# Kernel tuning notes

Hardware: AMD Instinct MI355X
Metric: run time of the kernel (lower is better)

## Reference

```python
import jax, jax.numpy as jnp
import numpy as np

N = 4096
D = 512   # d_model == dff (required by the original code path)
H = 4
NEG = -1e10
ALPHA = 0.3  # keras LeakyReLU default alpha


def setup_inputs() -> dict:
    key = jax.random.key(0)
    ks = jax.random.split(key, 8)
    nodes = jax.random.normal(ks[0], (N, D), dtype=jnp.float32)
    # sparse-ish 0/1 dense adjacency with self loops
    adj = (jax.random.uniform(ks[1], (N, N)) < 0.01).astype(jnp.float32)
    adj = jnp.maximum(adj, jnp.eye(N, dtype=jnp.float32))
    s = 0.05
    W_node = jax.random.normal(ks[2], (D, D), dtype=jnp.float32) * s
    b_node = jnp.zeros((D,), dtype=jnp.float32)
    K = jax.random.normal(ks[3], (H, D, D), dtype=jnp.float32) * s
    A_self = jax.random.normal(ks[4], (H, D), dtype=jnp.float32) * s
    A_neigh = jax.random.normal(ks[5], (H, D), dtype=jnp.float32) * s
    return {"nodes": nodes, "adj": adj, "W_node": W_node, "b_node": b_node,
            "K": K, "A_self": A_self, "A_neigh": A_neigh, "num_heads": H}


def reference(nodes, adj, W_node, b_node, K, A_self, A_neigh, num_heads):
    # node_layer: Dense(dff)
    x = nodes @ W_node + b_node                       # [N, D]
    # per-head projection, vectorized over heads
    feats = jnp.einsum('nd,hdf->hnf', x, K)           # [H, N, D]
    # additive attention scores; both terms are per-row scalars -> [H, N]
    s = jnp.einsum('hnf,hf->hn', feats, A_self) + jnp.einsum('hnf,hf->hn', feats, A_neigh)
    s = jnp.where(s > 0, s, ALPHA * s)                # LeakyReLU(alpha=0.3)
    # broadcast row score over columns + adjacency mask, softmax over neighbors
    logits = s[:, :, None] + NEG * (1.0 - adj)[None]  # [H, N, N]
    attn = jax.nn.softmax(logits, axis=-1)
    # dropout is identity at inference (training=False)
    out = jnp.einsum('hij,hjf->hif', attn, feats)     # [H, N, D]
    out = jnp.mean(out, axis=0)                       # mean over heads
    return jax.nn.relu(out)
```

## Files before the change

kernel.cpp:

```cpp
#include <hip/hip_runtime.h>


typedef short  short8 __attribute__((ext_vector_type(8)));
typedef float  f32x4  __attribute__((ext_vector_type(4)));

__device__ inline unsigned short f2bf(float f) {
    union { float f; unsigned int u; } v; v.f = f;
    unsigned int u = v.u;
    u += 0x7fffu + ((u >> 16) & 1u);
    return (unsigned short)(u >> 16);
}

__device__ inline void gl_lds16(const void* gp, void* lp) {
    __builtin_amdgcn_global_load_lds(
        (const __attribute__((address_space(1))) void*)gp,
        (__attribute__((address_space(3))) void*)lp, 16, 0, 0);
}

__global__ __launch_bounds__(256) void prep_kernel(
        const float* __restrict__ nodes, const float* __restrict__ adj,
        const float* __restrict__ W, const float* __restrict__ b,
        const float* __restrict__ K,
        unsigned short* __restrict__ MmatT, float* __restrict__ bias2,
        unsigned short* __restrict__ nodesBf,
        int* __restrict__ degArr, int* __restrict__ nbrArr,
        int N, int D, int H, int numCast) {
    __shared__ unsigned short As[64][32];
    __shared__ unsigned short Bs[64][32];
    __shared__ float red[4][64];
    __shared__ int lst[1024];
    __shared__ int cnt;

    const int bid = blockIdx.x;
    const int tid = threadIdx.x;
    const int DD  = D * D;
    const int lane = tid & 63, wave = tid >> 6;
    const int wy = wave >> 1, wx = wave & 1;
    const int l15 = lane & 15, quad = lane >> 4;

    if (bid < 64) {
        const int by = bid >> 3, bx = bid & 7;
        const int f0 = by * 64, d0 = bx * 64;
        const float invH = 1.0f / (float)H;
        const int kk = tid >> 3;
        const int ff = (tid & 7) * 8;
        const int dr = tid >> 2;
        const int dk = (tid & 3) * 8;
        f32x4 acc[2][2] = {};
        for (int k0 = 0; k0 < D; k0 += 32) {
            float s[8] = {0.f, 0.f, 0.f, 0.f, 0.f, 0.f, 0.f, 0.f};
            for (int h = 0; h < H; ++h) {
                const float* kp = K + ((size_t)h * D + (k0 + kk)) * D + f0 + ff;
                float4 x = *reinterpret_cast<const float4*>(kp);
                float4 y = *reinterpret_cast<const float4*>(kp + 4);
                s[0] += x.x; s[1] += x.y; s[2] += x.z; s[3] += x.w;
                s[4] += y.x; s[5] += y.y; s[6] += y.z; s[7] += y.w;
            }
            const float* wp = W + (size_t)(d0 + dr) * D + k0 + dk;
            float4 u = *reinterpret_cast<const float4*>(wp);
            float4 v = *reinterpret_cast<const float4*>(wp + 4);
            short8 bv;
            bv[0] = (short)f2bf(u.x); bv[1] = (short)f2bf(u.y);
            bv[2] = (short)f2bf(u.z); bv[3] = (short)f2bf(u.w);
            bv[4] = (short)f2bf(v.x); bv[5] = (short)f2bf(v.y);
            bv[6] = (short)f2bf(v.z); bv[7] = (short)f2bf(v.w);
            __syncthreads();
#pragma unroll
            for (int j = 0; j < 8; ++j)
                As[ff + j][kk] = f2bf(s[j] * invH);
            *reinterpret_cast<short8*>(&Bs[dr][dk]) = bv;
            __syncthreads();
            short8 a0 = *reinterpret_cast<const short8*>(&As[wy * 32 +      l15][quad * 8]);
            short8 a1 = *reinterpret_cast<const short8*>(&As[wy * 32 + 16 + l15][quad * 8]);
            short8 b0 = *reinterpret_cast<const short8*>(&Bs[wx * 32 +      l15][quad * 8]);
            short8 b1 = *reinterpret_cast<const short8*>(&Bs[wx * 32 + 16 + l15][quad * 8]);
            acc[0][0] = __builtin_amdgcn_mfma_f32_16x16x32_bf16(a0, b0, acc[0][0], 0, 0, 0);
            acc[0][1] = __builtin_amdgcn_mfma_f32_16x16x32_bf16(a0, b1, acc[0][1], 0, 0, 0);
            acc[1][0] = __builtin_amdgcn_mfma_f32_16x16x32_bf16(a1, b0, acc[1][0], 0, 0, 0);
            acc[1][1] = __builtin_amdgcn_mfma_f32_16x16x32_bf16(a1, b1, acc[1][1], 0, 0, 0);
        }
#pragma unroll
        for (int mi = 0; mi < 2; ++mi)
#pragma unroll
            for (int ni = 0; ni < 2; ++ni) {
                int col = d0 + wx * 32 + ni * 16 + l15;
#pragma unroll
                for (int r = 0; r < 4; ++r) {
                    int row = f0 + wy * 32 + mi * 16 + quad * 4 + r;
                    MmatT[(size_t)row * D + col] = f2bf(acc[mi][ni][r]);
                }
            }
    } else if (bid < 72) {
        const int f0 = (bid - 64) * 64;
        const int fl = tid & 63, grp = tid >> 6;
        const float invH = 1.0f / (float)H;
        float a = 0.f;
        for (int d = grp; d < D; d += 4) {
            const float* kp = K + (size_t)d * D + f0 + fl;
            float v = 0.f;
#pragma unroll
            for (int h = 0; h < 4; ++h) v += kp[(size_t)h * DD];
            a += b[d] * v;
        }
        red[grp][fl] = a;
        __syncthreads();
        if (tid < 64)
            bias2[f0 + tid] = (red[0][tid] + red[1][tid] + red[2][tid] + red[3][tid]) * invH;
    } else if (bid < 72 + N) {
        const int row = bid - 72;
        if (tid == 0) cnt = 0;
        __syncthreads();
        const float* arow = adj + (size_t)row * N;
        const int nper = N >> 8;
        const int base = tid * nper;
        const float4* ap = reinterpret_cast<const float4*>(arow + base);
        for (int c = 0; c < (nper >> 2); ++c) {
            float4 a = ap[c];
            int b4 = base + c * 4;
            if (a.x > 0.5f) { int p = atomicAdd(&cnt, 1); if (p < 1024) lst[p] = b4;     }
            if (a.y > 0.5f) { int p = atomicAdd(&cnt, 1); if (p < 1024) lst[p] = b4 + 1; }
            if (a.z > 0.5f) { int p = atomicAdd(&cnt, 1); if (p < 1024) lst[p] = b4 + 2; }
            if (a.w > 0.5f) { int p = atomicAdd(&cnt, 1); if (p < 1024) lst[p] = b4 + 3; }
        }
        __syncthreads();
        int deg = cnt; if (deg > 1024) deg = 1024;
        if (tid == 0) degArr[row] = deg;
        for (int i = tid; i < deg; i += 256)
            nbrArr[(size_t)row * 1024 + i] = lst[i];
    } else {
        const int total  = (N * D) >> 3;
        const int stride = numCast << 8;
        for (int i = (bid - 72 - N) * 256 + tid; i < total; i += stride) {
            const float* p = nodes + (size_t)i * 8;
            float4 x = *reinterpret_cast<const float4*>(p);
            float4 y = *reinterpret_cast<const float4*>(p + 4);
            short8 o;
            o[0] = (short)f2bf(x.x); o[1] = (short)f2bf(x.y);
            o[2] = (short)f2bf(x.z); o[3] = (short)f2bf(x.w);
            o[4] = (short)f2bf(y.x); o[5] = (short)f2bf(y.y);
            o[6] = (short)f2bf(y.z); o[7] = (short)f2bf(y.w);
            *reinterpret_cast<short8*>(nodesBf + (size_t)i * 8) = o;
        }
    }
}

__global__ __launch_bounds__(256) void gemm2_kernel(
        const unsigned short* __restrict__ nodesBf,
        const unsigned short* __restrict__ MmatT,
        const float* __restrict__ bias2, unsigned short* __restrict__ g, int D) {
    __shared__ unsigned short As[2][64][32];
    __shared__ unsigned short Bs[2][64][32];
    const int bid = blockIdx.x;
    const int by = bid >> 3, bx = bid & 7;
    const int tid = threadIdx.x;
    const int lane = tid & 63, wave = tid >> 6;
    const int wy = wave >> 1, wx = wave & 1;
    const int l15 = lane & 15, quad = lane >> 4;

    const unsigned short* Ag = nodesBf + (size_t)(by * 64 + (tid >> 2)) * D + (tid & 3) * 8;
    const unsigned short* Bg = MmatT   + (size_t)(bx * 64 + (tid >> 2)) * D + (tid & 3) * 8;
    unsigned short* AsW0 = &As[0][0][0] + wave * 512;
    unsigned short* AsW1 = &As[1][0][0] + wave * 512;
    unsigned short* BsW0 = &Bs[0][0][0] + wave * 512;
    unsigned short* BsW1 = &Bs[1][0][0] + wave * 512;

    f32x4 acc[2][2] = {};
    gl_lds16(Ag, AsW0);
    gl_lds16(Bg, BsW0);

    int cur = 0;
#pragma unroll
    for (int k0 = 0; k0 < 512; k0 += 32) {
        if (k0 + 32 < 512) {
            gl_lds16(Ag + k0 + 32, cur ? AsW0 : AsW1);
            gl_lds16(Bg + k0 + 32, cur ? BsW0 : BsW1);
            asm volatile("s_waitcnt vmcnt(2)" ::: "memory");
        } else {
            asm volatile("s_waitcnt vmcnt(0)" ::: "memory");
        }
        __builtin_amdgcn_s_barrier();
        __builtin_amdgcn_sched_barrier(0);
        const unsigned short (*A)[32] = cur ? As[1] : As[0];
        const unsigned short (*B)[32] = cur ? Bs[1] : Bs[0];
        short8 a0 = *reinterpret_cast<const short8*>(&A[wy * 32 +      l15][quad * 8]);
        short8 a1 = *reinterpret_cast<const short8*>(&A[wy * 32 + 16 + l15][quad * 8]);
        short8 b0 = *reinterpret_cast<const short8*>(&B[wx * 32 +      l15][quad * 8]);
        short8 b1 = *reinterpret_cast<const short8*>(&B[wx * 32 + 16 + l15][quad * 8]);
        acc[0][0] = __builtin_amdgcn_mfma_f32_16x16x32_bf16(a0, b0, acc[0][0], 0, 0, 0);
        acc[0][1] = __builtin_amdgcn_mfma_f32_16x16x32_bf16(a0, b1, acc[0][1], 0, 0, 0);
        acc[1][0] = __builtin_amdgcn_mfma_f32_16x16x32_bf16(a1, b0, acc[1][0], 0, 0, 0);
        acc[1][1] = __builtin_amdgcn_mfma_f32_16x16x32_bf16(a1, b1, acc[1][1], 0, 0, 0);
        __builtin_amdgcn_sched_barrier(0);
        asm volatile("s_waitcnt lgkmcnt(0)" ::: "memory");
        __builtin_amdgcn_s_barrier();
        cur ^= 1;
    }

#pragma unroll
    for (int mi = 0; mi < 2; ++mi)
#pragma unroll
        for (int ni = 0; ni < 2; ++ni) {
            int col = bx * 64 + wx * 32 + ni * 16 + l15;
            float bvl = bias2[col];
#pragma unroll
            for (int r = 0; r < 4; ++r) {
                int row = by * 64 + wy * 32 + mi * 16 + quad * 4 + r;
                g[(size_t)row * D + col] = f2bf(acc[mi][ni][r] + bvl);
            }
        }
}

__global__ __launch_bounds__(256) void aggregate_kernel(
        const int* __restrict__ degArr, const int* __restrict__ nbrArr,
        const unsigned short* __restrict__ g, float* __restrict__ out,
        int N, int D) {
    const int row = blockIdx.x;
    const int tid = threadIdx.x;
    __shared__ int lst[1024];
    const int deg = degArr[row];
    for (int i = tid; i < deg; i += 256) lst[i] = nbrArr[(size_t)row * 1024 + i];
    __syncthreads();

    const int col = tid * 2;
    float acc0 = 0.f, acc1 = 0.f;
    int k = 0;
    for (; k + 8 <= deg; k += 8) {
        unsigned int u[8];
#pragma unroll
        for (int j = 0; j < 8; ++j)
            u[j] = *reinterpret_cast<const unsigned int*>(&g[(size_t)lst[k + j] * D + col]);
#pragma unroll
        for (int j = 0; j < 8; ++j) {
            union { unsigned int i; float f; } lo, hi;
            lo.i = u[j] << 16; hi.i = u[j] & 0xffff0000u;
            acc0 += lo.f; acc1 += hi.f;
        }
    }
    for (; k < deg; ++k) {
        unsigned int u = *reinterpret_cast<const unsigned int*>(&g[(size_t)lst[k] * D + col]);
        union { unsigned int i; float f; } lo, hi;
        lo.i = u << 16; hi.i = u & 0xffff0000u;
        acc0 += lo.f; acc1 += hi.f;
    }

    float inv = deg > 0 ? 1.f / (float)deg : 0.f;
    acc0 *= inv; acc1 *= inv;
    float2 o;
    o.x = acc0 > 0.f ? acc0 : 0.f;
    o.y = acc1 > 0.f ? acc1 : 0.f;
    *reinterpret_cast<float2*>(&out[(size_t)row * D + col]) = o;
}

extern "C" void kernel_launch(void* const* d_in, const int* in_sizes, int n_in,
                              void* d_out, int out_size, void* d_ws, size_t ws_size,
                              hipStream_t stream) {
    const float* nodes  = (const float*)d_in[0];
    const float* adj    = (const float*)d_in[1];
    const float* W_node = (const float*)d_in[2];
    const float* b_node = (const float*)d_in[3];
    const float* K      = (const float*)d_in[4];

    const int D  = in_sizes[3];
    const int N  = in_sizes[0] / D;
    const int H  = in_sizes[4] / (D * D);
    const int DD = D * D;

    float* out = (float*)d_out;

    char* ws = (char*)d_ws;
    unsigned short* MmatT   = (unsigned short*)(ws);
    size_t off = (size_t)DD * 2;
    float*          bias2   = (float*)(ws + off);          off += (size_t)D * 4;
    unsigned short* nodesBf = (unsigned short*)(ws + off); off += (size_t)N * D * 2;
    unsigned short* g_bf16  = (unsigned short*)(ws + off); off += (size_t)N * D * 2;
    int*            degArr  = (int*)(ws + off);            off += (size_t)N * 4;
    int*            nbrArr  = (int*)(ws + off);

    const int numCast = 952;
    prep_kernel<<<dim3(64 + 8 + N + numCast), 256, 0, stream>>>(
        nodes, adj, W_node, b_node, K, MmatT, bias2, nodesBf, degArr, nbrArr,
        N, D, H, numCast);

    gemm2_kernel<<<dim3((N / 64) * (D / 64)), 256, 0, stream>>>(
        nodesBf, MmatT, bias2, g_bf16, D);

    aggregate_kernel<<<dim3(N), 256, 0, stream>>>(degArr, nbrArr, g_bf16, out, N, D);
}
```

Before: 168.2 us.

## Pad and swizzle LDS tiles, prefetch weights, coalesce adjacency scan, remap blocks

```diff
diff --git a/kernel.cpp b/kernel.cpp
--- a/kernel.cpp
+++ b/kernel.cpp
@@ -25,8 +25,8 @@
         unsigned short* __restrict__ nodesBf,
         int* __restrict__ degArr, int* __restrict__ nbrArr,
         int N, int D, int H, int numCast) {
-    __shared__ unsigned short As[64][32];
-    __shared__ unsigned short Bs[64][32];
+    __shared__ unsigned short As[64][40];
+    __shared__ unsigned short Bs[64][40];
     __shared__ float red[4][64];
     __shared__ int lst[1024];
     __shared__ int cnt;
@@ -46,24 +46,47 @@
         const int ff = (tid & 7) * 8;
         const int dr = tid >> 2;
         const int dk = (tid & 3) * 8;
+
+        float4 kc[4][2], wc[2];
+#pragma unroll
+        for (int h = 0; h < 4; ++h) {
+            const float* kp = K + ((size_t)h * D + kk) * D + f0 + ff;
+            kc[h][0] = *reinterpret_cast<const float4*>(kp);
+            kc[h][1] = *reinterpret_cast<const float4*>(kp + 4);
+        }
+        {
+            const float* wp = W + (size_t)(d0 + dr) * D + dk;
+            wc[0] = *reinterpret_cast<const float4*>(wp);
+            wc[1] = *reinterpret_cast<const float4*>(wp + 4);
+        }
+
         f32x4 acc[2][2] = {};
-        for (int k0 = 0; k0 < D; k0 += 32) {
-            float s[8] = {0.f, 0.f, 0.f, 0.f, 0.f, 0.f, 0.f, 0.f};
-            for (int h = 0; h < H; ++h) {
-                const float* kp = K + ((size_t)h * D + (k0 + kk)) * D + f0 + ff;
-                float4 x = *reinterpret_cast<const float4*>(kp);
-                float4 y = *reinterpret_cast<const float4*>(kp + 4);
-                s[0] += x.x; s[1] += x.y; s[2] += x.z; s[3] += x.w;
-                s[4] += y.x; s[5] += y.y; s[6] += y.z; s[7] += y.w;
-            }
-            const float* wp = W + (size_t)(d0 + dr) * D + k0 + dk;
-            float4 u = *reinterpret_cast<const float4*>(wp);
-            float4 v = *reinterpret_cast<const float4*>(wp + 4);
+#pragma unroll
+        for (int k0 = 0; k0 < 512; k0 += 32) {
+            float4 kn[4][2], wn[2];
+            if (k0 + 32 < 512) {
+#pragma unroll
+                for (int h = 0; h < 4; ++h) {
+                    const float* kp = K + ((size_t)h * D + (k0 + 32 + kk)) * D + f0 + ff;
+                    kn[h][0] = *reinterpret_cast<const float4*>(kp);
+                    kn[h][1] = *reinterpret_cast<const float4*>(kp + 4);
+                }
+                const float* wp = W + (size_t)(d0 + dr) * D + (k0 + 32) + dk;
+                wn[0] = *reinterpret_cast<const float4*>(wp);
+                wn[1] = *reinterpret_cast<const float4*>(wp + 4);
+            }
+            float s[8];
+#pragma unroll
+            for (int j = 0; j < 4; ++j) {
+                s[j]     = kc[0][0][j] + kc[1][0][j] + kc[2][0][j] + kc[3][0][j];
+                s[j + 4] = kc[0][1][j] + kc[1][1][j] + kc[2][1][j] + kc[3][1][j];
+            }
             short8 bv;
-            bv[0] = (short)f2bf(u.x); bv[1] = (short)f2bf(u.y);
-            bv[2] = (short)f2bf(u.z); bv[3] = (short)f2bf(u.w);
-            bv[4] = (short)f2bf(v.x); bv[5] = (short)f2bf(v.y);
-            bv[6] = (short)f2bf(v.z); bv[7] = (short)f2bf(v.w);
+#pragma unroll
+            for (int j = 0; j < 4; ++j) {
+                bv[j]     = (short)f2bf(wc[0][j]);
+                bv[j + 4] = (short)f2bf(wc[1][j]);
+            }
             __syncthreads();
 #pragma unroll
             for (int j = 0; j < 8; ++j)
@@ -78,6 +101,11 @@
             acc[0][1] = __builtin_amdgcn_mfma_f32_16x16x32_bf16(a0, b1, acc[0][1], 0, 0, 0);
             acc[1][0] = __builtin_amdgcn_mfma_f32_16x16x32_bf16(a1, b0, acc[1][0], 0, 0, 0);
             acc[1][1] = __builtin_amdgcn_mfma_f32_16x16x32_bf16(a1, b1, acc[1][1], 0, 0, 0);
+            if (k0 + 32 < 512) {
+#pragma unroll
+                for (int h = 0; h < 4; ++h) { kc[h][0] = kn[h][0]; kc[h][1] = kn[h][1]; }
+                wc[0] = wn[0]; wc[1] = wn[1];
+            }
         }
 #pragma unroll
         for (int mi = 0; mi < 2; ++mi)
@@ -110,17 +138,17 @@
         const int row = bid - 72;
         if (tid == 0) cnt = 0;
         __syncthreads();
-        const float* arow = adj + (size_t)row * N;
-        const int nper = N >> 8;
-        const int base = tid * nper;
-        const float4* ap = reinterpret_cast<const float4*>(arow + base);
-        for (int c = 0; c < (nper >> 2); ++c) {
-            float4 a = ap[c];
-            int b4 = base + c * 4;
-            if (a.x > 0.5f) { int p = atomicAdd(&cnt, 1); if (p < 1024) lst[p] = b4;     }
-            if (a.y > 0.5f) { int p = atomicAdd(&cnt, 1); if (p < 1024) lst[p] = b4 + 1; }
-            if (a.z > 0.5f) { int p = atomicAdd(&cnt, 1); if (p < 1024) lst[p] = b4 + 2; }
-            if (a.w > 0.5f) { int p = atomicAdd(&cnt, 1); if (p < 1024) lst[p] = b4 + 3; }
+        const float4* ap = reinterpret_cast<const float4*>(adj + (size_t)row * N);
+        float4 av[4];
+#pragma unroll
+        for (int c = 0; c < 4; ++c) av[c] = ap[c * 256 + tid];
+#pragma unroll
+        for (int c = 0; c < 4; ++c) {
+            int b4 = (c * 256 + tid) * 4;
+            if (av[c].x > 0.5f) { int p = atomicAdd(&cnt, 1); if (p < 1024) lst[p] = b4;     }
+            if (av[c].y > 0.5f) { int p = atomicAdd(&cnt, 1); if (p < 1024) lst[p] = b4 + 1; }
+            if (av[c].z > 0.5f) { int p = atomicAdd(&cnt, 1); if (p < 1024) lst[p] = b4 + 2; }
+            if (av[c].w > 0.5f) { int p = atomicAdd(&cnt, 1); if (p < 1024) lst[p] = b4 + 3; }
         }
         __syncthreads();
         int deg = cnt; if (deg > 1024) deg = 1024;
@@ -151,14 +179,16 @@
     __shared__ unsigned short As[2][64][32];
     __shared__ unsigned short Bs[2][64][32];
     const int bid = blockIdx.x;
-    const int by = bid >> 3, bx = bid & 7;
+    const int lb = (bid & 7) * 64 + (bid >> 3);
+    const int by = lb >> 3, bx = lb & 7;
     const int tid = threadIdx.x;
     const int lane = tid & 63, wave = tid >> 6;
     const int wy = wave >> 1, wx = wave & 1;
     const int l15 = lane & 15, quad = lane >> 4;
 
-    const unsigned short* Ag = nodesBf + (size_t)(by * 64 + (tid >> 2)) * D + (tid & 3) * 8;
-    const unsigned short* Bg = MmatT   + (size_t)(bx * 64 + (tid >> 2)) * D + (tid & 3) * 8;
+    const int cgl = ((tid & 3) ^ ((tid >> 3) & 3)) * 8;
+    const unsigned short* Ag = nodesBf + (size_t)(by * 64 + (tid >> 2)) * D + cgl;
+    const unsigned short* Bg = MmatT   + (size_t)(bx * 64 + (tid >> 2)) * D + cgl;
     unsigned short* AsW0 = &As[0][0][0] + wave * 512;
     unsigned short* AsW1 = &As[1][0][0] + wave * 512;
     unsigned short* BsW0 = &Bs[0][0][0] + wave * 512;
@@ -167,6 +197,10 @@
     f32x4 acc[2][2] = {};
     gl_lds16(Ag, AsW0);
     gl_lds16(Bg, BsW0);
+
+    const int ra = wy * 32 + l15, rb = wx * 32 + l15;
+    const int qa = (quad ^ ((ra >> 1) & 3)) * 8;
+    const int qb = (quad ^ ((rb >> 1) & 3)) * 8;
 
     int cur = 0;
 #pragma unroll
@@ -180,12 +214,12 @@
         }
         __builtin_amdgcn_s_barrier();
         __builtin_amdgcn_sched_barrier(0);
-        const unsigned short (*A)[32] = cur ? As[1] : As[0];
-        const unsigned short (*B)[32] = cur ? Bs[1] : Bs[0];
-        short8 a0 = *reinterpret_cast<const short8*>(&A[wy * 32 +      l15][quad * 8]);
-        short8 a1 = *reinterpret_cast<const short8*>(&A[wy * 32 + 16 + l15][quad * 8]);
-        short8 b0 = *reinterpret_cast<const short8*>(&B[wx * 32 +      l15][quad * 8]);
-        short8 b1 = *reinterpret_cast<const short8*>(&B[wx * 32 + 16 + l15][quad * 8]);
+        const unsigned short* Af = cur ? &As[1][0][0] : &As[0][0][0];
+        const unsigned short* Bf = cur ? &Bs[1][0][0] : &Bs[0][0][0];
+        short8 a0 = *reinterpret_cast<const short8*>(Af + (ra     ) * 32 + qa);
+        short8 a1 = *reinterpret_cast<const short8*>(Af + (ra + 16) * 32 + qa);
+        short8 b0 = *reinterpret_cast<const short8*>(Bf + (rb     ) * 32 + qb);
+        short8 b1 = *reinterpret_cast<const short8*>(Bf + (rb + 16) * 32 + qb);
         acc[0][0] = __builtin_amdgcn_mfma_f32_16x16x32_bf16(a0, b0, acc[0][0], 0, 0, 0);
         acc[0][1] = __builtin_amdgcn_mfma_f32_16x16x32_bf16(a0, b1, acc[0][1], 0, 0, 0);
         acc[1][0] = __builtin_amdgcn_mfma_f32_16x16x32_bf16(a1, b0, acc[1][0], 0, 0, 0);
```

Measured after the change: 158.6 us. 1.06x faster.
